# Performance work log

Hardware: AMD Instinct MI355X
Metric: run time of the kernel (lower is better)

The kernel has to match this reference:

```python
import jax, jax.numpy as jnp
import numpy as np
from jax import lax

B, H, W, C = 16, 56, 56, 256
NH = 8
KD = C // NH  # key/head dim = 32
FF = 1024
EPS = 1e-6
SCALE = KD ** -0.5


def _layernorm(x, g, b):
    m = jnp.mean(x, axis=-1, keepdims=True)
    v = jnp.mean(jnp.square(x - m), axis=-1, keepdims=True)
    return (x - m) * lax.rsqrt(v + EPS) * g + b


def _dwconv(x, w, b):
    # x: (B,H,W,Cd), w: (kh,kw,1,Cd) depthwise (groups = Cd), stride 1, SAME padding
    return lax.conv_general_dilated(
        x, w, window_strides=(1, 1), padding='SAME',
        dimension_numbers=('NHWC', 'HWIO', 'NHWC'),
        feature_group_count=x.shape[-1]) + b


def setup_inputs() -> dict:
    key = jax.random.key(0)
    ks = jax.random.split(key, 20)
    r = lambda i, shape, s=0.02: jax.random.normal(ks[i], shape, jnp.float32) * s
    return {
        'x': jax.random.normal(ks[0], (B, H, W, C), jnp.float32),
        'mask_h': jax.random.normal(ks[1], (NH, H, H), jnp.float32),
        'mask_w': jax.random.normal(ks[2], (NH, W, W), jnp.float32),
        # pos: DWConv2d(C, 3, 1, 1)
        'pos_w': r(3, (3, 3, 1, C)), 'pos_b': jnp.zeros((C,), jnp.float32),
        # retention layer norm
        'ln1_g': jnp.ones((C,), jnp.float32), 'ln1_b': jnp.zeros((C,), jnp.float32),
        # MaSA projections (stored as (in, out) so y = x @ W + b)
        'q_w': r(4, (C, C)), 'q_b': jnp.zeros((C,), jnp.float32),
        'k_w': r(5, (C, C)), 'k_b': jnp.zeros((C,), jnp.float32),
        'v_w': r(6, (C, C)), 'v_b': jnp.zeros((C,), jnp.float32),
        # lepe: DWConv2d(C, 5, 1, 2)
        'lepe_w': r(7, (5, 5, 1, C)), 'lepe_b': jnp.zeros((C,), jnp.float32),
        'out_w': r(8, (C, C)), 'out_b': jnp.zeros((C,), jnp.float32),
        # final layer norm
        'ln2_g': jnp.ones((C,), jnp.float32), 'ln2_b': jnp.zeros((C,), jnp.float32),
        # FFN
        'fc1_w': r(9, (C, FF)), 'fc1_b': jnp.zeros((FF,), jnp.float32),
        'fc2_w': r(10, (FF, C)), 'fc2_b': jnp.zeros((C,), jnp.float32),
    }


def _masa(x, mask_h, mask_w, q_w, q_b, k_w, k_b, v_w, v_b, lepe_w, lepe_b, out_w, out_b):
    b, h, w, _ = x.shape
    q = x @ q_w + q_b
    k = (x @ k_w + k_b) * SCALE
    v = x @ v_w + v_b
    lepe = _dwconv(v, lepe_w, lepe_b)
    qh = q.reshape(b, h, w, NH, KD)
    kh = k.reshape(b, h, w, NH, KD)
    vh = v.reshape(b, h, w, NH, KD)
    # width-axis retention: scores (b, h, NH, w, w), mask_w broadcasts as (NH, w, w)
    attn_w = jax.nn.softmax(jnp.einsum('bhqnd,bhknd->bhnqk', qh, kh) + mask_w, axis=-1)
    vw = jnp.einsum('bhnqk,bhknd->bhnqd', attn_w, vh)  # (b, h, NH, w, KD)
    # height-axis retention: scores (b, w, NH, h, h), mask_h broadcasts as (NH, h, h)
    attn_h = jax.nn.softmax(jnp.einsum('bqwnd,bkwnd->bwnqk', qh, kh) + mask_h, axis=-1)
    out = jnp.einsum('bwnqk,bknwd->bqwnd', attn_h, vw)  # (b, h, w, NH, KD)
    out = out.reshape(b, h, w, NH * KD) + lepe
    return out @ out_w + out_b


def reference(x, mask_h, mask_w, pos_w, pos_b, ln1_g, ln1_b,
              q_w, q_b, k_w, k_b, v_w, v_b, lepe_w, lepe_b, out_w, out_b,
              ln2_g, ln2_b, fc1_w, fc1_b, fc2_w, fc2_b):
    # RetBlock (retention='whole', no layerscale, no dropout / drop_path)
    x = x + _dwconv(x, pos_w, pos_b)
    x = x + _masa(_layernorm(x, ln1_g, ln1_b), mask_h, mask_w,
                  q_w, q_b, k_w, k_b, v_w, v_b, lepe_w, lepe_b, out_w, out_b)
    y = _layernorm(x, ln2_g, ln2_b)
    y = jax.nn.gelu(y @ fc1_w + fc1_b, approximate=False) @ fc2_w + fc2_b
    return x + y
```

## Files before the change

### kernel.cpp

```cpp
#include <hip/hip_runtime.h>
#include <hip/hip_bf16.h>
#include <math.h>
#include <stdint.h>

typedef __bf16 bf16;
typedef __bf16 bf16x8 __attribute__((ext_vector_type(8)));
typedef __bf16 bf16x4 __attribute__((ext_vector_type(4)));
typedef float f32x4 __attribute__((ext_vector_type(4)));

#define NPIX (16*56*56)
#define CH 256
#define SCALE_K 0.17677669529663687f

__device__ __forceinline__ float gelu_fast(float vv) {
    float t = vv * (-2.30220781f + -0.10294330f * vv * vv);
    float e = __builtin_amdgcn_exp2f(t);
    return vv * __builtin_amdgcn_rcpf(1.0f + e);
}

__global__ void wt_kernel(const float* __restrict__ w, float scale, int K, int N,
                          bf16* __restrict__ out)
{
    int total = K * N;
    for (int idx = blockIdx.x * blockDim.x + threadIdx.x; idx < total;
         idx += gridDim.x * blockDim.x) {
        int n = idx / K, k = idx - n * K;
        out[idx] = (bf16)(w[(size_t)k * N + n] * scale);
    }
}

__global__ void qkv_bias_kernel(const float* __restrict__ qb,
                                const float* __restrict__ kb,
                                const float* __restrict__ vb,
                                float* __restrict__ out)
{
    int i = blockIdx.x * blockDim.x + threadIdx.x;
    if (i < 256) out[i] = qb[i];
    else if (i < 512) out[i] = kb[i - 256] * SCALE_K;
    else if (i < 768) out[i] = vb[i - 512];
}

__global__ __launch_bounds__(256) void posconv_ln_kernel(
    const float* __restrict__ x, const float* __restrict__ w,
    const float* __restrict__ bias, const float* __restrict__ g,
    const float* __restrict__ bta, float* __restrict__ x1,
    bf16* __restrict__ tln)
{
    const int wave = threadIdx.x >> 6, lane = threadIdx.x & 63;
    const long pix = (long)blockIdx.x * 4 + wave;
    const int ww = (int)(pix % 56);
    const int hh = (int)((pix / 56) % 56);
    const int b  = (int)(pix / 3136);
    const int c  = lane * 4;
    float4 acc = ((const float4*)(bias + c))[0];
    float4 xin = ((const float4*)(x + pix * 256 + c))[0];
    acc.x += xin.x; acc.y += xin.y; acc.z += xin.z; acc.w += xin.w;
    #pragma unroll
    for (int dh = 0; dh < 3; ++dh) {
        int h2 = hh + dh - 1;
        if (h2 < 0 || h2 >= 56) continue;
        #pragma unroll
        for (int dw = 0; dw < 3; ++dw) {
            int w2 = ww + dw - 1;
            if (w2 < 0 || w2 >= 56) continue;
            float4 xv = ((const float4*)(x + (((long)(b * 56 + h2)) * 56 + w2) * 256 + c))[0];
            float4 wv = ((const float4*)(w + (dh * 3 + dw) * 256 + c))[0];
            acc.x += xv.x * wv.x; acc.y += xv.y * wv.y;
            acc.z += xv.z * wv.z; acc.w += xv.w * wv.w;
        }
    }
    ((float4*)(x1 + pix * 256 + c))[0] = acc;
    float s  = acc.x + acc.y + acc.z + acc.w;
    float q2 = acc.x * acc.x + acc.y * acc.y + acc.z * acc.z + acc.w * acc.w;
    #pragma unroll
    for (int o = 32; o; o >>= 1) {
        s  += __shfl_xor(s,  o, 64);
        q2 += __shfl_xor(q2, o, 64);
    }
    float mean = s * (1.0f / 256.0f);
    float var  = q2 * (1.0f / 256.0f) - mean * mean;
    float rs   = rsqrtf(var + 1e-6f);
    float4 gv = ((const float4*)g)[lane];
    float4 bv = ((const float4*)bta)[lane];
    bf16* o4 = tln + pix * 256 + c;
    o4[0] = (bf16)((acc.x - mean) * rs * gv.x + bv.x);
    o4[1] = (bf16)((acc.y - mean) * rs * gv.y + bv.y);
    o4[2] = (bf16)((acc.z - mean) * rs * gv.z + bv.z);
    o4[3] = (bf16)((acc.w - mean) * rs * gv.w + bv.w);
}

__global__ __launch_bounds__(256) void lepe_kernel(
    const bf16* __restrict__ qkv, const float* __restrict__ w,
    const float* __restrict__ bias, bf16* __restrict__ out)
{
    long idx = (long)blockIdx.x * 256 + threadIdx.x;
    int c8 = (int)(idx & 31);
    long pix = idx >> 5;
    int ww = (int)(pix % 56);
    int hh = (int)((pix / 56) % 56);
    int b  = (int)(pix / 3136);
    int c  = c8 * 8;
    float acc[8];
    #pragma unroll
    for (int j = 0; j < 8; ++j) acc[j] = bias[c + j];
    #pragma unroll
    for (int dh = 0; dh < 5; ++dh) {
        int h2 = hh + dh - 2;
        if (h2 < 0 || h2 >= 56) continue;
        #pragma unroll
        for (int dw = 0; dw < 5; ++dw) {
            int w2 = ww + dw - 2;
            if (w2 < 0 || w2 >= 56) continue;
            bf16x8 vv = *(const bf16x8*)(qkv + (((long)(b * 56 + h2)) * 56 + w2) * 768 + 512 + c);
            const float4* wp = (const float4*)(w + (dh * 5 + dw) * 256 + c);
            float4 w0 = wp[0], w1 = wp[1];
            acc[0] += (float)vv[0] * w0.x; acc[1] += (float)vv[1] * w0.y;
            acc[2] += (float)vv[2] * w0.z; acc[3] += (float)vv[3] * w0.w;
            acc[4] += (float)vv[4] * w1.x; acc[5] += (float)vv[5] * w1.y;
            acc[6] += (float)vv[6] * w1.z; acc[7] += (float)vv[7] * w1.w;
        }
    }
    bf16* o = out + pix * 256 + c;
    #pragma unroll
    for (int j = 0; j < 8; ++j) o[j] = (bf16)acc[j];
}

template<bool WIDTH>
__global__ __launch_bounds__(256) void attn_mfma_kernel(
    const bf16* __restrict__ qkv, const bf16* __restrict__ vsrc,
    const float* __restrict__ mask, const bf16* __restrict__ lepe,
    bf16* __restrict__ outp)
{
    __shared__ bf16 VtAll[4][32][72];
    __shared__ bf16 PlAll[4][16][72];
    const int tid = threadIdx.x;
    const int wave = tid >> 6, lane = tid & 63;
    const int g = lane >> 4, ql = lane & 15;
    const int n  = blockIdx.x / 224;
    const int s  = (blockIdx.x % 224) * 4 + wave;
    const int b  = s / 56, rc = s % 56;
    bf16 (*Vt)[72] = VtAll[wave];
    bf16 (*Pl)[72] = PlAll[wave];
    const long basePix = WIDTH ? ((long)(b * 56 + rc)) * 56 : (long)b * 3136 + rc;
    const long pixStride = WIDTH ? 1 : 56;
    const bf16* qb = qkv + basePix * 768 + n * 32;
    const long qstride = pixStride * 768;
    const bf16* vbp; long vstride;
    if (WIDTH) { vbp = qb + 512; vstride = qstride; }
    else       { vbp = vsrc + basePix * 256 + n * 32; vstride = pixStride * 256; }

    #pragma unroll
    for (int it = 0; it < 2; ++it) {
        int idx = it * 64 + lane;
        if (idx < 112) {
            int pp = idx >> 2, chunk = idx & 3;
            int pos0 = pp * 2;
            bf16x8 v0 = *(const bf16x8*)(vbp + (long)pos0 * vstride + chunk * 8);
            bf16x8 v1 = *(const bf16x8*)(vbp + (long)(pos0 + 1) * vstride + chunk * 8);
            int colb = pos0 ^ (chunk << 3);
            #pragma unroll
            for (int j = 0; j < 8; ++j) {
                union { bf16 h[2]; unsigned int u; } pk;
                pk.h[0] = v0[j]; pk.h[1] = v1[j];
                *(unsigned int*)&Vt[chunk * 8 + j][colb] = pk.u;
            }
        }
    }
    if (lane < 32) {
        int d = lane;
        int colb = 56 ^ ((d >> 3) << 3);
        *(float4*)&Vt[d][colb] = (float4){0.f, 0.f, 0.f, 0.f};
    }

    bf16x8 qf[4], kf[4];
    #pragma unroll
    for (int t4 = 0; t4 < 4; ++t4) {
        int row = ql + 16 * t4; if (row > 55) row = 55;
        qf[t4] = *(const bf16x8*)(qb + (long)row * qstride + 8 * g);
        kf[t4] = *(const bf16x8*)(qb + (long)row * qstride + 256 + 8 * g);
    }

    f32x4 sA[4][4];
    #pragma unroll
    for (int qt = 0; qt < 4; ++qt)
        #pragma unroll
        for (int kt = 0; kt < 4; ++kt)
            sA[qt][kt] = __builtin_amdgcn_mfma_f32_16x16x32_bf16(
                kf[kt], qf[qt], (f32x4){0.f, 0.f, 0.f, 0.f}, 0, 0, 0);

    const float* mrow = mask + n * 3136;
    #pragma unroll
    for (int qt = 0; qt < 4; ++qt) {
        int qm = ql + 16 * qt; if (qm > 55) qm = 55;
        #pragma unroll
        for (int kt = 0; kt < 4; ++kt) {
            if (kt == 3 && g >= 2) {
                sA[qt][3][0] = -3.0e38f; sA[qt][3][1] = -3.0e38f;
                sA[qt][3][2] = -3.0e38f; sA[qt][3][3] = -3.0e38f;
            } else {
                float4 mv = *(const float4*)(mrow + qm * 56 + kt * 16 + 4 * g);
                sA[qt][kt][0] += mv.x; sA[qt][kt][1] += mv.y;
                sA[qt][kt][2] += mv.z; sA[qt][kt][3] += mv.w;
            }
        }
    }

    #pragma unroll
    for (int qt = 0; qt < 4; ++qt) {
        float m = -3.0e38f;
        #pragma unroll
        for (int kt = 0; kt < 4; ++kt)
            #pragma unroll
            for (int r = 0; r < 4; ++r) m = fmaxf(m, sA[qt][kt][r]);
        m = fmaxf(m, __shfl_xor(m, 16, 64));
        m = fmaxf(m, __shfl_xor(m, 32, 64));
        float p[4][4];
        float sum = 0.f;
        #pragma unroll
        for (int kt = 0; kt < 4; ++kt)
            #pragma unroll
            for (int r = 0; r < 4; ++r) {
                float e = exp2f((sA[qt][kt][r] - m) * 1.4426950408889634f);
                p[kt][r] = e; sum += e;
            }
        sum += __shfl_xor(sum, 16, 64);
        sum += __shfl_xor(sum, 32, 64);
        float rinv = 1.0f / sum;
        #pragma unroll
        for (int kt = 0; kt < 4; ++kt) {
            bf16x4 w;
            #pragma unroll
            for (int r = 0; r < 4; ++r) w[r] = (bf16)(p[kt][r] * rinv);
            *(bf16x4*)&Pl[ql][kt * 16 + 4 * g] = w;
        }
        #pragma unroll
        for (int nt = 0; nt < 2; ++nt) {
            f32x4 o = {0.f, 0.f, 0.f, 0.f};
            #pragma unroll
            for (int ks = 0; ks < 2; ++ks) {
                bf16x8 af = *(const bf16x8*)&Pl[ql][ks * 32 + 8 * g];
                int vrow = ql + 16 * nt;
                int vcol = (ks * 32 + 8 * g) ^ ((vrow >> 3) << 3);
                bf16x8 bv = *(const bf16x8*)&Vt[vrow][vcol];
                o = __builtin_amdgcn_mfma_f32_16x16x32_bf16(af, bv, o, 0, 0, 0);
            }
            if (!(qt == 3 && g >= 2)) {
                #pragma unroll
                for (int r = 0; r < 4; ++r) {
                    int q = 16 * qt + 4 * g + r;
                    long addr = (basePix + (long)q * pixStride) * 256 + n * 32 + nt * 16 + ql;
                    float vv = o[r];
                    if (!WIDTH) vv += (float)lepe[addr];
                    outp[addr] = (bf16)vv;
                }
            }
        }
    }
}

template<bool GELU, bool RESID, bool OUT_BF16>
__global__ __launch_bounds__(256) void gemm_kernel(
    const bf16* __restrict__ A, const bf16* __restrict__ Wt,
    const float* __restrict__ bias, const float* __restrict__ resid,
    void* __restrict__ Cout, int M, int N, int K)
{
    __shared__ bf16 As[128 * 64];
    __shared__ bf16 Bs[128 * 64];
    const int t = threadIdx.x;
    const int wave = t >> 6, lane = t & 63;
    const int nTilesN = N >> 7;
    const int q8 = gridDim.x >> 3;
    const int o = ((int)blockIdx.x & 7) * q8 + ((int)blockIdx.x >> 3);
    const int tm = o / nTilesN, tn = o % nTilesN;
    const long m0 = (long)tm * 128, n0 = (long)tn * 128;
    const int waveM = (wave >> 1) * 64, waveN = (wave & 1) * 64;
    f32x4 acc[4][4] = {};

    for (int k0 = 0; k0 < K; k0 += 64) {
        #pragma unroll
        for (int i = 0; i < 4; ++i) {
            int c = i * 256 + wave * 64 + lane;
            int r = c >> 3, cc = (c & 7) * 8;
            const bf16* ga = A  + (m0 + r) * (long)K + k0 + cc;
            const bf16* gb = Wt + (n0 + r) * (long)K + k0 + cc;
            __builtin_amdgcn_global_load_lds(
                (const __attribute__((address_space(1))) void*)ga,
                (__attribute__((address_space(3))) void*)(As + (i * 256 + wave * 64) * 8),
                16, 0, 0);
            __builtin_amdgcn_global_load_lds(
                (const __attribute__((address_space(1))) void*)gb,
                (__attribute__((address_space(3))) void*)(Bs + (i * 256 + wave * 64) * 8),
                16, 0, 0);
        }
        __syncthreads();
        #pragma unroll
        for (int kk = 0; kk < 2; ++kk) {
            bf16x8 af[4], bfr[4];
            const int krow = kk * 32 + (lane >> 4) * 8;
            #pragma unroll
            for (int fm = 0; fm < 4; ++fm)
                af[fm] = *(const bf16x8*)&As[(waveM + fm * 16 + (lane & 15)) * 64 + krow];
            #pragma unroll
            for (int fn = 0; fn < 4; ++fn)
                bfr[fn] = *(const bf16x8*)&Bs[(waveN + fn * 16 + (lane & 15)) * 64 + krow];
            #pragma unroll
            for (int fm = 0; fm < 4; ++fm)
                #pragma unroll
                for (int fn = 0; fn < 4; ++fn)
                    acc[fm][fn] = __builtin_amdgcn_mfma_f32_16x16x32_bf16(
                        af[fm], bfr[fn], acc[fm][fn], 0, 0, 0);
        }
        __syncthreads();
    }

    #pragma unroll
    for (int fm = 0; fm < 4; ++fm) {
        #pragma unroll
        for (int r = 0; r < 4; ++r) {
            const long m = m0 + waveM + fm * 16 + (lane >> 4) * 4 + r;
            #pragma unroll
            for (int fn = 0; fn < 4; ++fn) {
                const long n = n0 + waveN + fn * 16 + (lane & 15);
                float vv = acc[fm][fn][r] + bias[n];
                if (GELU)  vv = gelu_fast(vv);
                if (RESID) vv += resid[m * N + n];
                if (OUT_BF16) ((bf16*)Cout)[m * N + n] = (bf16)vv;
                else          ((float*)Cout)[m * N + n] = vv;
            }
        }
    }
}

__global__ __launch_bounds__(256) void outln_kernel(
    const bf16* __restrict__ A, const bf16* __restrict__ Wt,
    const float* __restrict__ bias, const float* __restrict__ resid,
    const float* __restrict__ g2, const float* __restrict__ b2,
    float* __restrict__ x2out, bf16* __restrict__ uout)
{
    __shared__ bf16 As[64 * 64];
    __shared__ bf16 Bs[256 * 64];
    const int t = threadIdx.x;
    const int wave = t >> 6, lane = t & 63;
    const int g = lane >> 4, ql = lane & 15;
    const int q8 = gridDim.x >> 3;
    const int o = ((int)blockIdx.x & 7) * q8 + ((int)blockIdx.x >> 3);
    const long m0 = (long)o * 64;
    const int waveM = wave * 16;
    f32x4 acc[16] = {};

    for (int k0 = 0; k0 < 256; k0 += 64) {
        #pragma unroll
        for (int i = 0; i < 2; ++i) {
            int c = i * 256 + wave * 64 + lane;
            int r = c >> 3, cc = (c & 7) * 8;
            const bf16* ga = A + (m0 + r) * 256 + k0 + cc;
            __builtin_amdgcn_global_load_lds(
                (const __attribute__((address_space(1))) void*)ga,
                (__attribute__((address_space(3))) void*)(As + (i * 256 + wave * 64) * 8),
                16, 0, 0);
        }
        #pragma unroll
        for (int i = 0; i < 8; ++i) {
            int c = i * 256 + wave * 64 + lane;
            int r = c >> 3, cc = (c & 7) * 8;
            const bf16* gb = Wt + r * 256 + k0 + cc;
            __builtin_amdgcn_global_load_lds(
                (const __attribute__((address_space(1))) void*)gb,
                (__attribute__((address_space(3))) void*)(Bs + (i * 256 + wave * 64) * 8),
                16, 0, 0);
        }
        __syncthreads();
        #pragma unroll
        for (int kk = 0; kk < 2; ++kk) {
            const int krow = kk * 32 + g * 8;
            bf16x8 af = *(const bf16x8*)&As[(waveM + ql) * 64 + krow];
            #pragma unroll
            for (int fn = 0; fn < 16; ++fn) {
                bf16x8 bv = *(const bf16x8*)&Bs[(fn * 16 + ql) * 64 + krow];
                acc[fn] = __builtin_amdgcn_mfma_f32_16x16x32_bf16(af, bv, acc[fn], 0, 0, 0);
            }
        }
        __syncthreads();
    }

    float rsum[4] = {}, rsq[4] = {};
    #pragma unroll
    for (int fn = 0; fn < 16; ++fn) {
        const int n = fn * 16 + ql;
        const float bn = bias[n];
        #pragma unroll
        for (int r = 0; r < 4; ++r) {
            const long m = m0 + waveM + g * 4 + r;
            float v = acc[fn][r] + bn + resid[m * 256 + n];
            acc[fn][r] = v;
            rsum[r] += v; rsq[r] += v * v;
        }
    }
    #pragma unroll
    for (int r = 0; r < 4; ++r) {
        float s = rsum[r], q = rsq[r];
        #pragma unroll
        for (int off = 8; off; off >>= 1) {
            s += __shfl_xor(s, off, 64);
            q += __shfl_xor(q, off, 64);
        }
        float mean = s * (1.0f / 256.0f);
        float var  = q * (1.0f / 256.0f) - mean * mean;
        rsum[r] = mean;
        rsq[r]  = rsqrtf(var + 1e-6f);
    }
    #pragma unroll
    for (int fn = 0; fn < 16; ++fn) {
        const int n = fn * 16 + ql;
        const float gn = g2[n], bn2 = b2[n];
        #pragma unroll
        for (int r = 0; r < 4; ++r) {
            const long m = m0 + waveM + g * 4 + r;
            float v = acc[fn][r];
            x2out[m * 256 + n] = v;
            uout[m * 256 + n] = (bf16)((v - rsum[r]) * rsq[r] * gn + bn2);
        }
    }
}

extern "C" void kernel_launch(void* const* d_in, const int* in_sizes, int n_in,
                              void* d_out, int out_size, void* d_ws, size_t ws_size,
                              hipStream_t stream)
{
    (void)in_sizes; (void)n_in; (void)out_size; (void)ws_size;
    const float* x      = (const float*)d_in[0];
    const float* mask_h = (const float*)d_in[1];
    const float* mask_w = (const float*)d_in[2];
    const float* pos_w  = (const float*)d_in[3];
    const float* pos_b  = (const float*)d_in[4];
    const float* ln1_g  = (const float*)d_in[5];
    const float* ln1_b  = (const float*)d_in[6];
    const float* q_w    = (const float*)d_in[7];
    const float* q_b    = (const float*)d_in[8];
    const float* k_w    = (const float*)d_in[9];
    const float* k_b    = (const float*)d_in[10];
    const float* v_w    = (const float*)d_in[11];
    const float* v_b    = (const float*)d_in[12];
    const float* lepe_w = (const float*)d_in[13];
    const float* lepe_b = (const float*)d_in[14];
    const float* out_w  = (const float*)d_in[15];
    const float* out_b  = (const float*)d_in[16];
    const float* ln2_g  = (const float*)d_in[17];
    const float* ln2_b  = (const float*)d_in[18];
    const float* fc1_w  = (const float*)d_in[19];
    const float* fc1_b  = (const float*)d_in[20];
    const float* fc2_w  = (const float*)d_in[21];
    const float* fc2_b  = (const float*)d_in[22];

    char* ws = (char*)d_ws;
    size_t off = 0;
    auto alloc = [&](size_t bytes) -> void* {
        void* p = ws + off;
        off += (bytes + 255) & ~(size_t)255;
        return p;
    };
    const int M = NPIX;
    float* x1     = (float*)alloc((size_t)M * 256 * 4);
    bf16*  tln    = (bf16*) alloc((size_t)M * 256 * 2);
    bf16*  qkv    = (bf16*) alloc((size_t)M * 768 * 2);
    bf16*  lepeb  = (bf16*) alloc((size_t)M * 256 * 2);
    bf16*  vwb    = (bf16*) alloc((size_t)M * 256 * 2);
    bf16*  obuf   = (bf16*) alloc((size_t)M * 256 * 2);
    bf16*  wt_qkv = (bf16*) alloc((size_t)768 * 256 * 2);
    bf16*  wt_out = (bf16*) alloc((size_t)256 * 256 * 2);
    bf16*  wt_fc1 = (bf16*) alloc((size_t)1024 * 256 * 2);
    bf16*  wt_fc2 = (bf16*) alloc((size_t)256 * 1024 * 2);
    float* qkvb   = (float*)alloc(768 * 4);
    bf16*  h1     = tln;
    float* outf   = (float*)d_out;

    wt_kernel<<<256, 256, 0, stream>>>(q_w, 1.0f, 256, 256, wt_qkv);
    wt_kernel<<<256, 256, 0, stream>>>(k_w, SCALE_K, 256, 256, wt_qkv + 256 * 256);
    wt_kernel<<<256, 256, 0, stream>>>(v_w, 1.0f, 256, 256, wt_qkv + 512 * 256);
    wt_kernel<<<256, 256, 0, stream>>>(out_w, 1.0f, 256, 256, wt_out);
    wt_kernel<<<1024, 256, 0, stream>>>(fc1_w, 1.0f, 256, 1024, wt_fc1);
    wt_kernel<<<1024, 256, 0, stream>>>(fc2_w, 1.0f, 1024, 256, wt_fc2);
    qkv_bias_kernel<<<3, 256, 0, stream>>>(q_b, k_b, v_b, qkvb);

    posconv_ln_kernel<<<12544, 256, 0, stream>>>(x, pos_w, pos_b, ln1_g, ln1_b, x1, tln);
    gemm_kernel<false, false, true><<<392 * 6, 256, 0, stream>>>(
        tln, wt_qkv, qkvb, nullptr, qkv, M, 768, 256);
    lepe_kernel<<<6272, 256, 0, stream>>>(qkv, lepe_w, lepe_b, lepeb);
    attn_mfma_kernel<true><<<1792, 256, 0, stream>>>(qkv, nullptr, mask_w, nullptr, vwb);
    attn_mfma_kernel<false><<<1792, 256, 0, stream>>>(qkv, vwb, mask_h, lepeb, obuf);
    outln_kernel<<<784, 256, 0, stream>>>(
        obuf, wt_out, out_b, x1, ln2_g, ln2_b, outf, lepeb);
    gemm_kernel<true, false, true><<<392 * 8, 256, 0, stream>>>(
        lepeb, wt_fc1, fc1_b, nullptr, h1, M, 1024, 256);
    gemm_kernel<false, true, false><<<392 * 2, 256, 0, stream>>>(
        h1, wt_fc2, fc2_b, outf, outf, M, 256, 1024);
}
```

Baseline: 428.5 us.

## Fuse FFN fc1+GELU+fc2 into one kernel keeping hidden activations on-chip

Replaces the two FFN GEMM launches with a single fused kernel. Each 512-thread block owns 128 rows and streams fc1/fc2 weight chunks of 64 hidden units through XOR-swizzled LDS. The GELU hidden tile stays in per-wave LDS, and fc2 accumulates in registers before being added into the output. This removes the round trip of the M×1024 bf16 hidden tensor through global memory, at the cost of only 392 blocks, weights reloaded per block, and a large register footprint.

```diff
diff --git a/kernel.cpp b/kernel.cpp
--- a/kernel.cpp
+++ b/kernel.cpp
@@ -7,6 +7,9 @@
 typedef __bf16 bf16x8 __attribute__((ext_vector_type(8)));
 typedef __bf16 bf16x4 __attribute__((ext_vector_type(4)));
 typedef float f32x4 __attribute__((ext_vector_type(4)));
+
+#define AS1 __attribute__((address_space(1)))
+#define AS3 __attribute__((address_space(3)))
 
 #define NPIX (16*56*56)
 #define CH 256
@@ -284,13 +287,11 @@
             const bf16* ga = A  + (m0 + r) * (long)K + k0 + cc;
             const bf16* gb = Wt + (n0 + r) * (long)K + k0 + cc;
             __builtin_amdgcn_global_load_lds(
-                (const __attribute__((address_space(1))) void*)ga,
-                (__attribute__((address_space(3))) void*)(As + (i * 256 + wave * 64) * 8),
-                16, 0, 0);
+                (const AS1 void*)ga,
+                (AS3 void*)(As + (i * 256 + wave * 64) * 8), 16, 0, 0);
             __builtin_amdgcn_global_load_lds(
-                (const __attribute__((address_space(1))) void*)gb,
-                (__attribute__((address_space(3))) void*)(Bs + (i * 256 + wave * 64) * 8),
-                16, 0, 0);
+                (const AS1 void*)gb,
+                (AS3 void*)(Bs + (i * 256 + wave * 64) * 8), 16, 0, 0);
         }
         __syncthreads();
         #pragma unroll
@@ -355,9 +356,8 @@
             int r = c >> 3, cc = (c & 7) * 8;
             const bf16* ga = A + (m0 + r) * 256 + k0 + cc;
             __builtin_amdgcn_global_load_lds(
-                (const __attribute__((address_space(1))) void*)ga,
-                (__attribute__((address_space(3))) void*)(As + (i * 256 + wave * 64) * 8),
-                16, 0, 0);
+                (const AS1 void*)ga,
+                (AS3 void*)(As + (i * 256 + wave * 64) * 8), 16, 0, 0);
         }
         #pragma unroll
         for (int i = 0; i < 8; ++i) {
@@ -365,9 +365,8 @@
             int r = c >> 3, cc = (c & 7) * 8;
             const bf16* gb = Wt + r * 256 + k0 + cc;
             __builtin_amdgcn_global_load_lds(
-                (const __attribute__((address_space(1))) void*)gb,
-                (__attribute__((address_space(3))) void*)(Bs + (i * 256 + wave * 64) * 8),
-                16, 0, 0);
+                (const AS1 void*)gb,
+                (AS3 void*)(Bs + (i * 256 + wave * 64) * 8), 16, 0, 0);
         }
         __syncthreads();
         #pragma unroll
@@ -419,6 +418,99 @@
             float v = acc[fn][r];
             x2out[m * 256 + n] = v;
             uout[m * 256 + n] = (bf16)((v - rsum[r]) * rsq[r] * gn + bn2);
+        }
+    }
+}
+
+__global__ __launch_bounds__(512) void ffn_kernel(
+    const bf16* __restrict__ u, const bf16* __restrict__ w1t,
+    const float* __restrict__ b1, const bf16* __restrict__ w2t,
+    const float* __restrict__ b2, float* __restrict__ outf)
+{
+    __shared__ bf16 w1[64 * 256];
+    __shared__ bf16 w2[256 * 64];
+    __shared__ bf16 hAll[8][16 * 64];
+    const int t = threadIdx.x;
+    const int wid = t >> 6, lane = t & 63;
+    const int g = lane >> 4, ql = lane & 15;
+    const int q8 = gridDim.x >> 3;
+    const int o = ((int)blockIdx.x & 7) * q8 + ((int)blockIdx.x >> 3);
+    const long mb = (long)o * 128 + wid * 16;
+    bf16* hls = hAll[wid];
+
+    bf16x8 aq[8];
+    #pragma unroll
+    for (int kt = 0; kt < 8; ++kt)
+        aq[kt] = *(const bf16x8*)(u + (mb + ql) * 256 + kt * 32 + g * 8);
+
+    f32x4 acc2[16] = {};
+
+    for (int c = 0; c < 16; ++c) {
+        __syncthreads();
+        #pragma unroll
+        for (int i = 0; i < 4; ++i) {
+            int s = i * 512 + t;
+            int n = s >> 5, kc = s & 31;
+            const bf16* src = w1t + (c * 64 + n) * 256 + ((kc ^ (n & 7)) * 8);
+            __builtin_amdgcn_global_load_lds(
+                (const AS1 void*)src, (AS3 void*)(w1 + s * 8), 16, 0, 0);
+        }
+        #pragma unroll
+        for (int i = 0; i < 4; ++i) {
+            int s = i * 512 + t;
+            int n = s >> 3, kc = s & 7;
+            const bf16* src = w2t + n * 1024 + c * 64 + ((kc ^ (n & 7)) * 8);
+            __builtin_amdgcn_global_load_lds(
+                (const AS1 void*)src, (AS3 void*)(w2 + s * 8), 16, 0, 0);
+        }
+        __syncthreads();
+
+        f32x4 acc1[4] = {};
+        #pragma unroll
+        for (int fn = 0; fn < 4; ++fn) {
+            int n = fn * 16 + ql;
+            #pragma unroll
+            for (int kt = 0; kt < 8; ++kt) {
+                bf16x8 wf = *(const bf16x8*)&w1[(n * 32 + ((kt * 4 + g) ^ (n & 7))) * 8];
+                acc1[fn] = __builtin_amdgcn_mfma_f32_16x16x32_bf16(
+                    aq[kt], wf, acc1[fn], 0, 0, 0);
+            }
+        }
+        #pragma unroll
+        for (int fn = 0; fn < 4; ++fn) {
+            int col = fn * 16 + ql;
+            float bb = b1[c * 64 + col];
+            #pragma unroll
+            for (int r = 0; r < 4; ++r) {
+                int row = g * 4 + r;
+                float hv = gelu_fast(acc1[fn][r] + bb);
+                hls[row * 64 + (((col >> 3) ^ (row & 7)) * 8) + (col & 7)] = (bf16)hv;
+            }
+        }
+        bf16x8 hf[2];
+        #pragma unroll
+        for (int kkt = 0; kkt < 2; ++kkt)
+            hf[kkt] = *(const bf16x8*)&hls[ql * 64 + (((kkt * 4 + g) ^ (ql & 7)) * 8)];
+        #pragma unroll
+        for (int fn = 0; fn < 16; ++fn) {
+            int n = fn * 16 + ql;
+            #pragma unroll
+            for (int kkt = 0; kkt < 2; ++kkt) {
+                bf16x8 wf = *(const bf16x8*)&w2[(n * 8 + ((kkt * 4 + g) ^ (n & 7))) * 8];
+                acc2[fn] = __builtin_amdgcn_mfma_f32_16x16x32_bf16(
+                    hf[kkt], wf, acc2[fn], 0, 0, 0);
+            }
+        }
+    }
+
+    #pragma unroll
+    for (int fn = 0; fn < 16; ++fn) {
+        int n = fn * 16 + ql;
+        float bb = b2[n];
+        #pragma unroll
+        for (int r = 0; r < 4; ++r) {
+            long row = mb + g * 4 + r;
+            outf[row * 256 + n] += acc2[fn][r] + bb;
         }
     }
 }
@@ -471,7 +563,6 @@
     bf16*  wt_fc1 = (bf16*) alloc((size_t)1024 * 256 * 2);
     bf16*  wt_fc2 = (bf16*) alloc((size_t)256 * 1024 * 2);
     float* qkvb   = (float*)alloc(768 * 4);
-    bf16*  h1     = tln;
     float* outf   = (float*)d_out;
 
     wt_kernel<<<256, 256, 0, stream>>>(q_w, 1.0f, 256, 256, wt_qkv);
@@ -490,8 +581,6 @@
     attn_mfma_kernel<false><<<1792, 256, 0, stream>>>(qkv, vwb, mask_h, lepeb, obuf);
     outln_kernel<<<784, 256, 0, stream>>>(
         obuf, wt_out, out_b, x1, ln2_g, ln2_b, outf, lepeb);
-    gemm_kernel<true, false, true><<<392 * 8, 256, 0, stream>>>(
-        lepeb, wt_fc1, fc1_b, nullptr, h1, M, 1024, 256);
-    gemm_kernel<false, true, false><<<392 * 2, 256, 0, stream>>>(
-        h1, wt_fc2, fc2_b, outf, outf, M, 256, 1024);
-}
+    ffn_kernel<<<392, 512, 0, stream>>>(
+        lepeb, wt_fc1, fc1_b, wt_fc2, fc2_b, outf);
+}
```

Result: no change. 436.5 us (+1.9%).

## Merge weight prep into one kernel and make GEMMs persistent with capped grids

Applied to the files above, without the earlier changes.

The six weight-transpose launches and the bias-packing launch are replaced by a single prep kernel that converts and transposes all weights and biases, which cuts launch overhead. The GEMM kernel becomes a grid-stride persistent loop over tiles, and the QKV and FC1 launches are capped at 1280 blocks. This reduces block scheduling overhead and the tail effect, at the cost of less even load balance when the tile count does not divide the grid evenly.

```diff
diff --git a/kernel.cpp b/kernel.cpp
--- a/kernel.cpp
+++ b/kernel.cpp
@@ -8,6 +8,9 @@
 typedef __bf16 bf16x4 __attribute__((ext_vector_type(4)));
 typedef float f32x4 __attribute__((ext_vector_type(4)));
 
+#define AS1 __attribute__((address_space(1)))
+#define AS3 __attribute__((address_space(3)))
+
 #define NPIX (16*56*56)
 #define CH 256
 #define SCALE_K 0.17677669529663687f
@@ -18,26 +21,37 @@
     return vv * __builtin_amdgcn_rcpf(1.0f + e);
 }
 
-__global__ void wt_kernel(const float* __restrict__ w, float scale, int K, int N,
-                          bf16* __restrict__ out)
-{
-    int total = K * N;
-    for (int idx = blockIdx.x * blockDim.x + threadIdx.x; idx < total;
-         idx += gridDim.x * blockDim.x) {
-        int n = idx / K, k = idx - n * K;
-        out[idx] = (bf16)(w[(size_t)k * N + n] * scale);
-    }
-}
-
-__global__ void qkv_bias_kernel(const float* __restrict__ qb,
-                                const float* __restrict__ kb,
-                                const float* __restrict__ vb,
-                                float* __restrict__ out)
-{
-    int i = blockIdx.x * blockDim.x + threadIdx.x;
-    if (i < 256) out[i] = qb[i];
-    else if (i < 512) out[i] = kb[i - 256] * SCALE_K;
-    else if (i < 768) out[i] = vb[i - 512];
+__global__ __launch_bounds__(256) void prep_kernel(
+    const float* __restrict__ q_w, const float* __restrict__ k_w,
+    const float* __restrict__ v_w, const float* __restrict__ out_w,
+    const float* __restrict__ fc1_w, const float* __restrict__ fc2_w,
+    const float* __restrict__ qb, const float* __restrict__ kb,
+    const float* __restrict__ vb,
+    bf16* __restrict__ wt_qkv, bf16* __restrict__ wt_out,
+    bf16* __restrict__ wt_fc1, bf16* __restrict__ wt_fc2,
+    float* __restrict__ qkvb)
+{
+    int idx = blockIdx.x * 256 + threadIdx.x;
+    if (idx < 262144) {
+        int w = idx >> 16;
+        int j = idx & 65535;
+        int n = j >> 8, k = j & 255;
+        const float* src = (w == 0) ? q_w : (w == 1) ? k_w : (w == 2) ? v_w : out_w;
+        float scale = (w == 1) ? SCALE_K : 1.0f;
+        bf16* dst = (w < 3) ? (wt_qkv + w * 65536) : wt_out;
+        dst[j] = (bf16)(src[k * 256 + n] * scale);
+    } else if (idx < 524288) {
+        int j = idx - 262144;
+        int n = j >> 8, k = j & 255;
+        wt_fc1[j] = (bf16)(fc1_w[k * 1024 + n]);
+    } else if (idx < 786432) {
+        int j = idx - 524288;
+        int n = j >> 10, k = j & 1023;
+        wt_fc2[j] = (bf16)(fc2_w[k * 256 + n]);
+    } else if (idx < 787200) {
+        int i = idx - 786432;
+        qkvb[i] = (i < 256) ? qb[i] : (i < 512) ? kb[i - 256] * SCALE_K : vb[i - 512];
+    }
 }
 
 __global__ __launch_bounds__(256) void posconv_ln_kernel(
@@ -269,63 +283,65 @@
     const int t = threadIdx.x;
     const int wave = t >> 6, lane = t & 63;
     const int nTilesN = N >> 7;
-    const int q8 = gridDim.x >> 3;
-    const int o = ((int)blockIdx.x & 7) * q8 + ((int)blockIdx.x >> 3);
-    const int tm = o / nTilesN, tn = o % nTilesN;
-    const long m0 = (long)tm * 128, n0 = (long)tn * 128;
+    const int nTiles = (M >> 7) * nTilesN;
+    const int q8 = nTiles >> 3;
     const int waveM = (wave >> 1) * 64, waveN = (wave & 1) * 64;
-    f32x4 acc[4][4] = {};
-
-    for (int k0 = 0; k0 < K; k0 += 64) {
-        #pragma unroll
-        for (int i = 0; i < 4; ++i) {
-            int c = i * 256 + wave * 64 + lane;
-            int r = c >> 3, cc = (c & 7) * 8;
-            const bf16* ga = A  + (m0 + r) * (long)K + k0 + cc;
-            const bf16* gb = Wt + (n0 + r) * (long)K + k0 + cc;
-            __builtin_amdgcn_global_load_lds(
-                (const __attribute__((address_space(1))) void*)ga,
-                (__attribute__((address_space(3))) void*)(As + (i * 256 + wave * 64) * 8),
-                16, 0, 0);
-            __builtin_amdgcn_global_load_lds(
-                (const __attribute__((address_space(1))) void*)gb,
-                (__attribute__((address_space(3))) void*)(Bs + (i * 256 + wave * 64) * 8),
-                16, 0, 0);
-        }
-        __syncthreads();
-        #pragma unroll
-        for (int kk = 0; kk < 2; ++kk) {
-            bf16x8 af[4], bfr[4];
-            const int krow = kk * 32 + (lane >> 4) * 8;
-            #pragma unroll
-            for (int fm = 0; fm < 4; ++fm)
-                af[fm] = *(const bf16x8*)&As[(waveM + fm * 16 + (lane & 15)) * 64 + krow];
-            #pragma unroll
-            for (int fn = 0; fn < 4; ++fn)
-                bfr[fn] = *(const bf16x8*)&Bs[(waveN + fn * 16 + (lane & 15)) * 64 + krow];
-            #pragma unroll
-            for (int fm = 0; fm < 4; ++fm)
+
+    for (int gidx = blockIdx.x; gidx < nTiles; gidx += gridDim.x) {
+        const int o = (gidx & 7) * q8 + (gidx >> 3);
+        const int tm = o / nTilesN, tn = o % nTilesN;
+        const long m0 = (long)tm * 128, n0 = (long)tn * 128;
+        f32x4 acc[4][4] = {};
+
+        for (int k0 = 0; k0 < K; k0 += 64) {
+            #pragma unroll
+            for (int i = 0; i < 4; ++i) {
+                int c = i * 256 + wave * 64 + lane;
+                int r = c >> 3, cc = (c & 7) * 8;
+                const bf16* ga = A  + (m0 + r) * (long)K + k0 + cc;
+                const bf16* gb = Wt + (n0 + r) * (long)K + k0 + cc;
+                __builtin_amdgcn_global_load_lds(
+                    (const AS1 void*)ga,
+                    (AS3 void*)(As + (i * 256 + wave * 64) * 8), 16, 0, 0);
+                __builtin_amdgcn_global_load_lds(
+                    (const AS1 void*)gb,
+                    (AS3 void*)(Bs + (i * 256 + wave * 64) * 8), 16, 0, 0);
+            }
+            __syncthreads();
+            #pragma unroll
+            for (int kk = 0; kk < 2; ++kk) {
+                bf16x8 af[4], bfr[4];
+                const int krow = kk * 32 + (lane >> 4) * 8;
+                #pragma unroll
+                for (int fm = 0; fm < 4; ++fm)
+                    af[fm] = *(const bf16x8*)&As[(waveM + fm * 16 + (lane & 15)) * 64 + krow];
                 #pragma unroll
                 for (int fn = 0; fn < 4; ++fn)
-                    acc[fm][fn] = __builtin_amdgcn_mfma_f32_16x16x32_bf16(
-                        af[fm], bfr[fn], acc[fm][fn], 0, 0, 0);
-        }
-        __syncthreads();
-    }
-
-    #pragma unroll
-    for (int fm = 0; fm < 4; ++fm) {
-        #pragma unroll
-        for (int r = 0; r < 4; ++r) {
-            const long m = m0 + waveM + fm * 16 + (lane >> 4) * 4 + r;
-            #pragma unroll
-            for (int fn = 0; fn < 4; ++fn) {
-                const long n = n0 + waveN + fn * 16 + (lane & 15);
-                float vv = acc[fm][fn][r] + bias[n];
-                if (GELU)  vv = gelu_fast(vv);
-                if (RESID) vv += resid[m * N + n];
-                if (OUT_BF16) ((bf16*)Cout)[m * N + n] = (bf16)vv;
-                else          ((float*)Cout)[m * N + n] = vv;
+                    bfr[fn] = *(const bf16x8*)&Bs[(waveN + fn * 16 + (lane & 15)) * 64 + krow];
+                #pragma unroll
+                for (int fm = 0; fm < 4; ++fm)
+                    #pragma unroll
+                    for (int fn = 0; fn < 4; ++fn)
+                        acc[fm][fn] = __builtin_amdgcn_mfma_f32_16x16x32_bf16(
+                            af[fm], bfr[fn], acc[fm][fn], 0, 0, 0);
+            }
+            __syncthreads();
+        }
+
+        #pragma unroll
+        for (int fm = 0; fm < 4; ++fm) {
+            #pragma unroll
+            for (int r = 0; r < 4; ++r) {
+                const long m = m0 + waveM + fm * 16 + (lane >> 4) * 4 + r;
+                #pragma unroll
+                for (int fn = 0; fn < 4; ++fn) {
+                    const long n = n0 + waveN + fn * 16 + (lane & 15);
+                    float vv = acc[fm][fn][r] + bias[n];
+                    if (GELU)  vv = gelu_fast(vv);
+                    if (RESID) vv += resid[m * N + n];
+                    if (OUT_BF16) ((bf16*)Cout)[m * N + n] = (bf16)vv;
+                    else          ((float*)Cout)[m * N + n] = vv;
+                }
             }
         }
     }
@@ -355,9 +371,8 @@
             int r = c >> 3, cc = (c & 7) * 8;
             const bf16* ga = A + (m0 + r) * 256 + k0 + cc;
             __builtin_amdgcn_global_load_lds(
-                (const __attribute__((address_space(1))) void*)ga,
-                (__attribute__((address_space(3))) void*)(As + (i * 256 + wave * 64) * 8),
-                16, 0, 0);
+                (const AS1 void*)ga,
+                (AS3 void*)(As + (i * 256 + wave * 64) * 8), 16, 0, 0);
         }
         #pragma unroll
         for (int i = 0; i < 8; ++i) {
@@ -365,9 +380,8 @@
             int r = c >> 3, cc = (c & 7) * 8;
             const bf16* gb = Wt + r * 256 + k0 + cc;
             __builtin_amdgcn_global_load_lds(
-                (const __attribute__((address_space(1))) void*)gb,
-                (__attribute__((address_space(3))) void*)(Bs + (i * 256 + wave * 64) * 8),
-                16, 0, 0);
+                (const AS1 void*)gb,
+                (AS3 void*)(Bs + (i * 256 + wave * 64) * 8), 16, 0, 0);
         }
         __syncthreads();
         #pragma unroll
@@ -474,24 +488,20 @@
     bf16*  h1     = tln;
     float* outf   = (float*)d_out;
 
-    wt_kernel<<<256, 256, 0, stream>>>(q_w, 1.0f, 256, 256, wt_qkv);
-    wt_kernel<<<256, 256, 0, stream>>>(k_w, SCALE_K, 256, 256, wt_qkv + 256 * 256);
-    wt_kernel<<<256, 256, 0, stream>>>(v_w, 1.0f, 256, 256, wt_qkv + 512 * 256);
-    wt_kernel<<<256, 256, 0, stream>>>(out_w, 1.0f, 256, 256, wt_out);
-    wt_kernel<<<1024, 256, 0, stream>>>(fc1_w, 1.0f, 256, 1024, wt_fc1);
-    wt_kernel<<<1024, 256, 0, stream>>>(fc2_w, 1.0f, 1024, 256, wt_fc2);
-    qkv_bias_kernel<<<3, 256, 0, stream>>>(q_b, k_b, v_b, qkvb);
+    prep_kernel<<<3075, 256, 0, stream>>>(
+        q_w, k_w, v_w, out_w, fc1_w, fc2_w, q_b, k_b, v_b,
+        wt_qkv, wt_out, wt_fc1, wt_fc2, qkvb);
 
     posconv_ln_kernel<<<12544, 256, 0, stream>>>(x, pos_w, pos_b, ln1_g, ln1_b, x1, tln);
-    gemm_kernel<false, false, true><<<392 * 6, 256, 0, stream>>>(
+    gemm_kernel<false, false, true><<<1280, 256, 0, stream>>>(
         tln, wt_qkv, qkvb, nullptr, qkv, M, 768, 256);
     lepe_kernel<<<6272, 256, 0, stream>>>(qkv, lepe_w, lepe_b, lepeb);
     attn_mfma_kernel<true><<<1792, 256, 0, stream>>>(qkv, nullptr, mask_w, nullptr, vwb);
     attn_mfma_kernel<false><<<1792, 256, 0, stream>>>(qkv, vwb, mask_h, lepeb, obuf);
     outln_kernel<<<784, 256, 0, stream>>>(
         obuf, wt_out, out_b, x1, ln2_g, ln2_b, outf, lepeb);
-    gemm_kernel<true, false, true><<<392 * 8, 256, 0, stream>>>(
+    gemm_kernel<true, false, true><<<1280, 256, 0, stream>>>(
         lepeb, wt_fc1, fc1_b, nullptr, h1, M, 1024, 256);
-    gemm_kernel<false, true, false><<<392 * 2, 256, 0, stream>>>(
+    gemm_kernel<false, true, false><<<784, 256, 0, stream>>>(
         h1, wt_fc2, fc2_b, outf, outf, M, 256, 1024);
 }
```

Result: slower. 471.4 us (+10.0%).
